# Optimization experiments

Measured on AMD Instinct MI355X. Metric: run time of the kernel, lower is better.

Reference implementation:

```python
import jax, jax.numpy as jnp
import numpy as np


def setup_inputs() -> dict:
    key = jax.random.key(0)
    ks = jax.random.split(key, 8)
    B, H, W, C = 4, 64, 64, 64
    Cf = C // 8
    x = jax.random.normal(ks[0], (B, H, W, C), dtype=jnp.float32)
    # 1x1 conv kernels stored as [C_in, C_out] (kernel_size=1)
    w_f = jax.random.normal(ks[1], (C, Cf), dtype=jnp.float32) * 0.05
    b_f = jax.random.normal(ks[2], (Cf,), dtype=jnp.float32) * 0.05
    w_g = jax.random.normal(ks[3], (C, Cf), dtype=jnp.float32) * 0.05
    b_g = jax.random.normal(ks[4], (Cf,), dtype=jnp.float32) * 0.05
    w_h = jax.random.normal(ks[5], (C, C), dtype=jnp.float32) * 0.05
    b_h = jax.random.normal(ks[6], (C,), dtype=jnp.float32) * 0.05
    gamma = jax.random.normal(ks[7], (1,), dtype=jnp.float32) * 0.1
    return {"x": x, "w_f": w_f, "b_f": b_f, "w_g": w_g, "b_g": b_g,
            "w_h": w_h, "b_h": b_h, "gamma": gamma}


def reference(x, w_f, b_f, w_g, b_g, w_h, b_h, gamma):
    B, H, W, C = x.shape
    N = H * W
    xf = x.reshape(B, N, C)  # 1x1 conv == per-pixel linear
    f = xf @ w_f + b_f       # [B, N, C/8]
    g = xf @ w_g + b_g       # [B, N, C/8]
    h = xf @ w_h + b_h       # [B, N, C]
    # attention_map[b, i, j] = <g_i, f_j>, softmax over last axis
    scores = jnp.einsum('bic,bjc->bij', g, f)  # [B, N, N]
    attn = jax.nn.softmax(scores, axis=-1)
    out = jnp.einsum('bij,bjc->bic', attn, h)  # [B, N, C]
    out = out.reshape(B, H, W, C)
    return gamma * out + x
```

## Files before the change

### kernel.cpp

```cpp
#include <hip/hip_runtime.h>
#include <hip/hip_bf16.h>

typedef __bf16 bf16;
typedef __bf16 bf16x8 __attribute__((ext_vector_type(8)));
typedef __bf16 bf16x4 __attribute__((ext_vector_type(4)));
typedef float floatx4 __attribute__((ext_vector_type(4)));

typedef int    aint    __attribute__((may_alias));
typedef long   along   __attribute__((may_alias));
typedef float4 afloat4 __attribute__((may_alias));

#define NPIX 4096
#define BATCH 4
#define LOG2E 1.4426950408889634f

__device__ inline bf16x8 zero8() {
    bf16x8 v;
    #pragma unroll
    for (int i = 0; i < 8; ++i) v[i] = (bf16)0.0f;
    return v;
}

__global__ __launch_bounds__(256) void proj_kernel(
    const float* __restrict__ x,
    const float* __restrict__ w_f, const float* __restrict__ b_f,
    const float* __restrict__ w_g, const float* __restrict__ b_g,
    const float* __restrict__ w_h, const float* __restrict__ b_h,
    bf16* __restrict__ fq, bf16* __restrict__ gq, unsigned char* __restrict__ hT)
{
    __shared__ bf16 xs[64 * 72];
    __shared__ bf16 wt[80 * 72];
    __shared__ float bs[80];
    const int tid = threadIdx.x;
    const int p0 = blockIdx.x * 64;

    {
        const float4* xg = (const float4*)(x + (long)p0 * 64);
        #pragma unroll
        for (int it = 0; it < 4; ++it) {
            int i4 = tid + it * 256;
            float4 v = xg[i4];
            int row = i4 >> 4, c4 = (i4 & 15) * 4;
            bf16x4 pk;
            pk[0] = (bf16)v.x; pk[1] = (bf16)v.y; pk[2] = (bf16)v.z; pk[3] = (bf16)v.w;
            *(bf16x4*)(&xs[row * 72 + c4]) = pk;
        }
    }
    for (int idx = tid; idx < 80 * 64; idx += 256) {
        int n = idx >> 6, c = idx & 63;
        float v = (n < 8) ? w_f[c * 8 + n]
                : (n < 16) ? w_g[c * 8 + (n - 8)]
                : w_h[c * 64 + (n - 16)];
        wt[n * 72 + c] = (bf16)v;
    }
    if (tid < 80)
        bs[tid] = (tid < 8) ? b_f[tid] : (tid < 16) ? b_g[tid - 8] : b_h[tid - 16];
    __syncthreads();

    const int wv = tid >> 6, lane = tid & 63;
    const int quad = lane >> 4, l15 = lane & 15;
    const int b = blockIdx.x >> 6;
    const int n0pix = (p0 & (NPIX - 1)) + wv * 16 + quad * 4;

    bf16x8 a0 = *(const bf16x8*)(&xs[(wv * 16 + l15) * 72 + quad * 8]);
    bf16x8 a1 = *(const bf16x8*)(&xs[(wv * 16 + l15) * 72 + 32 + quad * 8]);

    #pragma unroll
    for (int nt = 0; nt < 5; ++nt) {
        float bias = bs[nt * 16 + l15];
        floatx4 acc = {bias, bias, bias, bias};
        bf16x8 b0 = *(const bf16x8*)(&wt[(nt * 16 + l15) * 72 + quad * 8]);
        bf16x8 b1 = *(const bf16x8*)(&wt[(nt * 16 + l15) * 72 + 32 + quad * 8]);
        acc = __builtin_amdgcn_mfma_f32_16x16x32_bf16(a0, b0, acc, 0, 0, 0);
        acc = __builtin_amdgcn_mfma_f32_16x16x32_bf16(a1, b1, acc, 0, 0, 0);
        if (nt == 0) {
            #pragma unroll
            for (int r = 0; r < 4; ++r) {
                long P = (long)p0 + wv * 16 + quad * 4 + r;
                if (l15 < 8) fq[P * 8 + l15] = (bf16)acc[r];
                else         gq[P * 8 + (l15 - 8)] = (bf16)(acc[r] * LOG2E);
            }
        } else {
            int c = nt * 16 + l15 - 16;
            int pk = __builtin_amdgcn_cvt_pk_fp8_f32(acc[0], acc[1], 0, false);
            pk     = __builtin_amdgcn_cvt_pk_fp8_f32(acc[2], acc[3], pk, true);
            *(aint*)(hT + ((long)b * 64 + c) * NPIX + n0pix) = pk;
        }
    }
}

#define FBASE 0
#define HBASE 4096
#define PBASE 20480
#define LDSTOT 29184

__global__ __launch_bounds__(256) void attn_kernel(
    const bf16* __restrict__ fq, const bf16* __restrict__ gq,
    const unsigned char* __restrict__ hT, float* __restrict__ partial)
{
    __shared__ char smem[LDSTOT];
    const int tid  = threadIdx.x;
    const int wv   = tid >> 6, lane = tid & 63;
    const int quad = lane >> 4, l15 = lane & 15;
    const int js   = blockIdx.x >> 8;
    const int ib   = blockIdx.x & 255;
    const int b    = ib >> 6, it = ib & 63;
    const long rowbase = (long)b * NPIX + it * 64 + wv * 16;
    const int jbase = js * 1024;

    bf16x8 gfrag = zero8();
    if (lane < 16) gfrag = *(const bf16x8*)(gq + (rowbase + lane) * 8);

    const char* gp[3]; int lo[3], dlt[3], gstep[3]; bool act[3];
    #pragma unroll
    for (int k = 0; k < 3; ++k) {
        int ch = k * 256 + tid;
        act[k] = (ch < 640);
        if (ch < 128) {
            lo[k]   = FBASE + ch * 16;
            dlt[k]  = 2048;
            gp[k]   = (const char*)fq + ((long)b * NPIX + jbase) * 16 + ch * 16;
            gstep[k] = 128 * 16;
        } else {
            int q = (ch - 128) & 511;
            int c = q >> 3, u = q & 7;
            lo[k]   = HBASE + c * 128 + ((u ^ (c & 7)) << 4);
            dlt[k]  = 8192;
            gp[k]   = (const char*)hT + ((long)b * 64 + c) * NPIX + jbase + u * 16;
            gstep[k] = 128;
        }
    }

    floatx4 acc[5];
    #pragma unroll
    for (int nt = 0; nt < 5; ++nt) acc[nt] = (floatx4){0.f, 0.f, 0.f, 0.f};
    const along ones = 0x3838383838383838L;
    char* Pw = smem + PBASE + wv * 2176;

    #pragma unroll
    for (int k = 0; k < 3; ++k)
        if (act[k]) {
            *(afloat4*)(smem + lo[k]) = *(const float4*)gp[k];
            gp[k] += gstep[k];
        }
    __syncthreads();

    for (int t = 0; t < 8; ++t) {
        const int buf = t & 1;
        float4 pre[3];
        if (t < 7) {
            #pragma unroll
            for (int k = 0; k < 3; ++k)
                if (act[k]) { pre[k] = *(const float4*)gp[k]; gp[k] += gstep[k]; }
        }
        const char* Fb = smem + FBASE + buf * 2048;
        const char* Hb = smem + HBASE + buf * 8192;

        #pragma unroll
        for (int j8 = 0; j8 < 8; ++j8) {
            bf16x8 afrag = zero8();
            if (lane < 16) afrag = *(const bf16x8*)(Fb + (j8 * 16 + l15) * 16);
            floatx4 s = __builtin_amdgcn_mfma_f32_16x16x32_bf16(
                afrag, gfrag, (floatx4){0.f, 0.f, 0.f, 0.f}, 0, 0, 0);
            float e0 = __builtin_amdgcn_exp2f(s[0]);
            float e1 = __builtin_amdgcn_exp2f(s[1]);
            float e2 = __builtin_amdgcn_exp2f(s[2]);
            float e3 = __builtin_amdgcn_exp2f(s[3]);
            int pk = __builtin_amdgcn_cvt_pk_fp8_f32(e0, e1, 0, false);
            pk     = __builtin_amdgcn_cvt_pk_fp8_f32(e2, e3, pk, true);
            *(aint*)(Pw + l15 * 136 + j8 * 16 + quad * 4) = pk;
        }
        asm volatile("" ::: "memory");
        #pragma unroll
        for (int ks = 0; ks < 4; ++ks) {
            along pfrag = *(const along*)(Pw + l15 * 136 + ks * 32 + quad * 8);
            #pragma unroll
            for (int nt = 0; nt < 4; ++nt) {
                int row = nt * 16 + l15;
                int unit = 2 * ks + (quad >> 1);
                along bfrag = *(const along*)(Hb + row * 128
                              + ((unit ^ (row & 7)) << 4) + (quad & 1) * 8);
                acc[nt] = __builtin_amdgcn_mfma_f32_16x16x32_fp8_fp8(pfrag, bfrag, acc[nt], 0, 0, 0);
            }
            acc[4] = __builtin_amdgcn_mfma_f32_16x16x32_fp8_fp8(pfrag, ones, acc[4], 0, 0, 0);
        }
        __syncthreads();
        if (t < 7) {
            #pragma unroll
            for (int k = 0; k < 3; ++k)
                if (act[k])
                    *(afloat4*)(smem + lo[k] + (buf ^ 1) * dlt[k]) = pre[k];
        }
        __syncthreads();
    }

    float* pb = partial + ((long)js * (BATCH * NPIX) + rowbase) * 68;
    #pragma unroll
    for (int nt = 0; nt < 4; ++nt)
        #pragma unroll
        for (int r = 0; r < 4; ++r)
            pb[(quad * 4 + r) * 68 + nt * 16 + l15] = acc[nt][r];
    if (l15 == 0) {
        #pragma unroll
        for (int r = 0; r < 4; ++r)
            pb[(quad * 4 + r) * 68 + 64] = acc[4][r];
    }
}

__global__ __launch_bounds__(256) void reduce_kernel(
    const float* __restrict__ partial, const float* __restrict__ x,
    const float* __restrict__ gamma_p, float* __restrict__ out)
{
    const int tid = threadIdx.x;
    const long i  = (long)blockIdx.x * 32 + (tid >> 3);
    const int c0  = (tid & 7) * 8;
    const float* p = partial + i * 68;
    float4 n0 = {0.f, 0.f, 0.f, 0.f}, n1 = {0.f, 0.f, 0.f, 0.f};
    float den = 0.f;
    #pragma unroll
    for (int js = 0; js < 4; ++js) {
        const float* pj = p + (long)js * (BATCH * NPIX) * 68;
        float4 a = *(const float4*)(pj + c0);
        float4 c = *(const float4*)(pj + c0 + 4);
        n0.x += a.x; n0.y += a.y; n0.z += a.z; n0.w += a.w;
        n1.x += c.x; n1.y += c.y; n1.z += c.z; n1.w += c.w;
        den += pj[64];
    }
    const float rd = gamma_p[0] / den;
    const float* xr = x + i * 64 + c0;
    float* orow = out + i * 64 + c0;
    float4 xa = *(const float4*)xr, xb = *(const float4*)(xr + 4);
    float4 oa, ob;
    oa.x = n0.x * rd + xa.x; oa.y = n0.y * rd + xa.y;
    oa.z = n0.z * rd + xa.z; oa.w = n0.w * rd + xa.w;
    ob.x = n1.x * rd + xb.x; ob.y = n1.y * rd + xb.y;
    ob.z = n1.z * rd + xb.z; ob.w = n1.w * rd + xb.w;
    *(float4*)orow = oa; *(float4*)(orow + 4) = ob;
}

extern "C" void kernel_launch(void* const* d_in, const int* in_sizes, int n_in,
                              void* d_out, int out_size, void* d_ws, size_t ws_size,
                              hipStream_t stream) {
    const float* x     = (const float*)d_in[0];
    const float* w_f   = (const float*)d_in[1];
    const float* b_f   = (const float*)d_in[2];
    const float* w_g   = (const float*)d_in[3];
    const float* b_g   = (const float*)d_in[4];
    const float* w_h   = (const float*)d_in[5];
    const float* b_h   = (const float*)d_in[6];
    const float* gamma = (const float*)d_in[7];
    float* out = (float*)d_out;

    bf16* fq = (bf16*)d_ws;
    bf16* gq = fq + 16384 * 8;
    unsigned char* hT = (unsigned char*)(gq + 16384 * 8);
    float* partial = (float*)(hT + (long)BATCH * 64 * NPIX);

    proj_kernel<<<256, 256, 0, stream>>>(x, w_f, b_f, w_g, b_g, w_h, b_h, fq, gq, hT);
    attn_kernel<<<1024, 256, 0, stream>>>(fq, gq, hT, partial);
    reduce_kernel<<<512, 256, 0, stream>>>(partial, x, gamma, out);
}
```

Baseline: 113.9 us.

## Retile hT layout and load F/H fragments directly from global, dropping LDS staging

The projection kernel now writes the fp8 h tensor in 32-pixel tiles, with each tile holding all 64 channels contiguously. This lets the attention kernel load B fragments straight from global memory into registers. The double-buffered LDS staging of F and H and both per-iteration block barriers are removed, so LDS now holds only the per-wave P scratch. In exchange, each wave reads H and F from global/L2 with no sharing across the four waves in a block, which raises cache traffic and exposes load latency without explicit prefetch.

```diff
diff --git a/kernel.cpp b/kernel.cpp
--- a/kernel.cpp
+++ b/kernel.cpp
@@ -8,11 +8,11 @@
 
 typedef int    aint    __attribute__((may_alias));
 typedef long   along   __attribute__((may_alias));
-typedef float4 afloat4 __attribute__((may_alias));
 
 #define NPIX 4096
 #define BATCH 4
 #define LOG2E 1.4426950408889634f
+#define HT_BATCH 262144
 
 __device__ inline bf16x8 zero8() {
     bf16x8 v;
@@ -84,21 +84,17 @@
             int c = nt * 16 + l15 - 16;
             int pk = __builtin_amdgcn_cvt_pk_fp8_f32(acc[0], acc[1], 0, false);
             pk     = __builtin_amdgcn_cvt_pk_fp8_f32(acc[2], acc[3], pk, true);
-            *(aint*)(hT + ((long)b * 64 + c) * NPIX + n0pix) = pk;
-        }
-    }
-}
-
-#define FBASE 0
-#define HBASE 4096
-#define PBASE 20480
-#define LDSTOT 29184
+            *(aint*)(hT + (long)b * HT_BATCH + (n0pix >> 5) * 2048
+                     + c * 32 + (n0pix & 31)) = pk;
+        }
+    }
+}
 
 __global__ __launch_bounds__(256) void attn_kernel(
     const bf16* __restrict__ fq, const bf16* __restrict__ gq,
     const unsigned char* __restrict__ hT, float* __restrict__ partial)
 {
-    __shared__ char smem[LDSTOT];
+    __shared__ char smem[4 * 2176];
     const int tid  = threadIdx.x;
     const int wv   = tid >> 6, lane = tid & 63;
     const int quad = lane >> 4, l15 = lane & 15;
@@ -111,55 +107,27 @@
     bf16x8 gfrag = zero8();
     if (lane < 16) gfrag = *(const bf16x8*)(gq + (rowbase + lane) * 8);
 
-    const char* gp[3]; int lo[3], dlt[3], gstep[3]; bool act[3];
-    #pragma unroll
-    for (int k = 0; k < 3; ++k) {
-        int ch = k * 256 + tid;
-        act[k] = (ch < 640);
-        if (ch < 128) {
-            lo[k]   = FBASE + ch * 16;
-            dlt[k]  = 2048;
-            gp[k]   = (const char*)fq + ((long)b * NPIX + jbase) * 16 + ch * 16;
-            gstep[k] = 128 * 16;
-        } else {
-            int q = (ch - 128) & 511;
-            int c = q >> 3, u = q & 7;
-            lo[k]   = HBASE + c * 128 + ((u ^ (c & 7)) << 4);
-            dlt[k]  = 8192;
-            gp[k]   = (const char*)hT + ((long)b * 64 + c) * NPIX + jbase + u * 16;
-            gstep[k] = 128;
-        }
-    }
+    const bf16* Fb = fq + ((long)b * NPIX + jbase) * 8;
+    const unsigned char* Hb = hT + (long)b * HT_BATCH + (jbase >> 5) * 2048
+                            + (l15 * 32 + quad * 8);
 
     floatx4 acc[5];
     #pragma unroll
     for (int nt = 0; nt < 5; ++nt) acc[nt] = (floatx4){0.f, 0.f, 0.f, 0.f};
     const along ones = 0x3838383838383838L;
-    char* Pw = smem + PBASE + wv * 2176;
-
-    #pragma unroll
-    for (int k = 0; k < 3; ++k)
-        if (act[k]) {
-            *(afloat4*)(smem + lo[k]) = *(const float4*)gp[k];
-            gp[k] += gstep[k];
-        }
-    __syncthreads();
+    char* Pw = smem + wv * 2176;
 
     for (int t = 0; t < 8; ++t) {
-        const int buf = t & 1;
-        float4 pre[3];
-        if (t < 7) {
+        along bfr[16];
+        #pragma unroll
+        for (int ks = 0; ks < 4; ++ks)
             #pragma unroll
-            for (int k = 0; k < 3; ++k)
-                if (act[k]) { pre[k] = *(const float4*)gp[k]; gp[k] += gstep[k]; }
-        }
-        const char* Fb = smem + FBASE + buf * 2048;
-        const char* Hb = smem + HBASE + buf * 8192;
-
+            for (int nt = 0; nt < 4; ++nt)
+                bfr[ks * 4 + nt] = *(const along*)(Hb + (t * 4 + ks) * 2048 + nt * 512);
         #pragma unroll
         for (int j8 = 0; j8 < 8; ++j8) {
             bf16x8 afrag = zero8();
-            if (lane < 16) afrag = *(const bf16x8*)(Fb + (j8 * 16 + l15) * 16);
+            if (lane < 16) afrag = *(const bf16x8*)(Fb + (t * 128 + j8 * 16 + l15) * 8);
             floatx4 s = __builtin_amdgcn_mfma_f32_16x16x32_bf16(
                 afrag, gfrag, (floatx4){0.f, 0.f, 0.f, 0.f}, 0, 0, 0);
             float e0 = __builtin_amdgcn_exp2f(s[0]);
@@ -175,23 +143,11 @@
         for (int ks = 0; ks < 4; ++ks) {
             along pfrag = *(const along*)(Pw + l15 * 136 + ks * 32 + quad * 8);
             #pragma unroll
-            for (int nt = 0; nt < 4; ++nt) {
-                int row = nt * 16 + l15;
-                int unit = 2 * ks + (quad >> 1);
-                along bfrag = *(const along*)(Hb + row * 128
-                              + ((unit ^ (row & 7)) << 4) + (quad & 1) * 8);
-                acc[nt] = __builtin_amdgcn_mfma_f32_16x16x32_fp8_fp8(pfrag, bfrag, acc[nt], 0, 0, 0);
-            }
+            for (int nt = 0; nt < 4; ++nt)
+                acc[nt] = __builtin_amdgcn_mfma_f32_16x16x32_fp8_fp8(
+                    pfrag, bfr[ks * 4 + nt], acc[nt], 0, 0, 0);
             acc[4] = __builtin_amdgcn_mfma_f32_16x16x32_fp8_fp8(pfrag, ones, acc[4], 0, 0, 0);
         }
-        __syncthreads();
-        if (t < 7) {
-            #pragma unroll
-            for (int k = 0; k < 3; ++k)
-                if (act[k])
-                    *(afloat4*)(smem + lo[k] + (buf ^ 1) * dlt[k]) = pre[k];
-        }
-        __syncthreads();
     }
 
     float* pb = partial + ((long)js * (BATCH * NPIX) + rowbase) * 68;
@@ -254,7 +210,7 @@
     bf16* fq = (bf16*)d_ws;
     bf16* gq = fq + 16384 * 8;
     unsigned char* hT = (unsigned char*)(gq + 16384 * 8);
-    float* partial = (float*)(hT + (long)BATCH * 64 * NPIX);
+    float* partial = (float*)(hT + (long)BATCH * HT_BATCH);
 
     proj_kernel<<<256, 256, 0, stream>>>(x, w_f, b_f, w_g, b_g, w_h, b_h, fq, gq, hT);
     attn_kernel<<<1024, 256, 0, stream>>>(fq, gq, hT, partial);
```

After: 118.1 us. +3.7%, slower.
